# Optimization experiments

Hardware: AMD Instinct MI355X
Metric: run time of the kernel (lower is better)

Reference implementation:

```python
import jax, jax.numpy as jnp
import numpy as np

B, C, H, W = 16, 192, 56, 56
WS = 7; L = WS * WS; NH = 8; HD = C // NH
SHIFTS = (0, 3, 0, 3)  # shift = 0 if i%2==0 else window_size//2


def _ln(x, g, b):
    m = jnp.mean(x, -1, keepdims=True)
    v = jnp.var(x, -1, keepdims=True)
    return (x - m) * jax.lax.rsqrt(v + 1e-5) * g + b


def _win_part(x):
    # (b, H, W, c) -> (b*nW, L, c)
    b, c = x.shape[0], x.shape[-1]
    x = x.reshape(b, H // WS, WS, W // WS, WS, c).transpose(0, 1, 3, 2, 4, 5)
    return x.reshape(-1, L, c)


def _win_rev(xw, b):
    # (b*nW, L, c) -> (b, H, W, c)
    c = xw.shape[-1]
    x = xw.reshape(b, H // WS, W // WS, WS, WS, c).transpose(0, 1, 3, 2, 4, 5)
    return x.reshape(b, H, W, c)


def _rel_index():
    co = np.stack(np.meshgrid(np.arange(WS), np.arange(WS), indexing='ij')).reshape(2, -1)
    r = (co[:, :, None] - co[:, None, :]).transpose(1, 2, 0).astype(np.int64)
    r[..., 0] += WS - 1; r[..., 1] += WS - 1; r[..., 0] *= 2 * WS - 1
    return r.sum(-1)  # (L, L)

REL_IDX = _rel_index()


def _mask(shift):
    if shift == 0:
        return None
    img = np.zeros((1, H, W, 1), np.float32)
    cnt = 0.0
    sl = (slice(0, H - WS), slice(H - WS, H - shift), slice(H - shift, None))
    for hs in sl:
        for ws_ in sl:
            img[:, hs, ws_, :] = cnt
            cnt += 1.0
    mw = np.asarray(_win_part(jnp.asarray(img))).reshape(-1, L)
    am = mw[:, None, :] - mw[:, :, None]
    return jnp.asarray(np.where(am != 0, -100.0, 0.0).astype(np.float32))  # (nW, L, L)

MASKS = [_mask(s) for s in SHIFTS]


def _block(x, n1g, n1b, qw, qb, pw, pb, tab, n2g, n2b, f1w, f1b, f2w, f2b, shift, mask):
    b = x.shape[0]
    sc = x
    x = _ln(x, n1g, n1b)
    if shift:
        x = jnp.roll(x, (-shift, -shift), (1, 2))
    xw = _win_part(x)  # (b*nW, L, C)
    qkv = (xw @ qw.T + qb).reshape(-1, L, 3, NH, HD).transpose(2, 0, 3, 1, 4)
    q, k, v = qkv[0], qkv[1], qkv[2]  # (nB, NH, L, HD)
    attn = jnp.einsum('bhid,bhjd->bhij', q * (HD ** -0.5), k)
    attn = attn + tab[REL_IDX].transpose(2, 0, 1)  # relative position bias (NH, L, L)
    if mask is not None:
        nW = mask.shape[0]
        attn = (attn.reshape(b, nW, NH, L, L) + mask[None, :, None]).reshape(-1, NH, L, L)
    attn = jax.nn.softmax(attn, -1)
    out = jnp.einsum('bhij,bhjd->bhid', attn, v).transpose(0, 2, 1, 3).reshape(-1, L, C)
    out = out @ pw.T + pb
    x = _win_rev(out, b)
    if shift:
        x = jnp.roll(x, (shift, shift), (1, 2))
    x = sc + x
    y = _ln(x, n2g, n2b)
    y = jax.nn.gelu(y @ f1w.T + f1b, approximate=False) @ f2w.T + f2b
    return x + y


def _conv_bn_relu(x, w, b, g, bt, m, v):
    x = jax.lax.conv_general_dilated(x, w, (1, 1), ((1, 1), (1, 1)),
                                     dimension_numbers=('NCHW', 'OIHW', 'NCHW'))
    x = x + b[None, :, None, None]
    x = (x - m[None, :, None, None]) * jax.lax.rsqrt(v + 1e-5)[None, :, None, None]
    x = x * g[None, :, None, None] + bt[None, :, None, None]
    return jax.nn.relu(x)


def setup_inputs() -> dict:
    key = jax.random.key(0)
    ks = iter(jax.random.split(key, 48))
    rn = lambda shape, s=0.02: jax.random.normal(next(ks), shape, jnp.float32) * s
    OD = 96
    return dict(
        x=jax.random.normal(next(ks), (B, C, H, W), jnp.float32),
        pos_embed=rn((1, H * W, C)),
        proj_w=rn((C, C)), proj_b=jnp.zeros((C,)),
        pe_g=jnp.ones((C,)), pe_b=jnp.zeros((C,)),
        n1_g=jnp.ones((4, C)), n1_b=jnp.zeros((4, C)),
        qkv_w=rn((4, 3 * C, C)), qkv_b=jnp.zeros((4, 3 * C)),
        attn_pw=rn((4, C, C)), attn_pb=jnp.zeros((4, C)),
        rel_tab=rn((4, (2 * WS - 1) ** 2, NH)),
        n2_g=jnp.ones((4, C)), n2_b=jnp.zeros((4, C)),
        fc1_w=rn((4, 4 * C, C)), fc1_b=jnp.zeros((4, 4 * C)),
        fc2_w=rn((4, C, 4 * C)), fc2_b=jnp.zeros((4, C)),
        c1_w=rn((C, C, 3, 3)), c1_b=jnp.zeros((C,)),
        bn1_g=jnp.ones((C,)), bn1_b=jnp.zeros((C,)), bn1_m=rn((C,), 0.1), bn1_v=jnp.ones((C,)),
        c2_w=rn((OD, C, 3, 3)), c2_b=jnp.zeros((OD,)),
        bn2_g=jnp.ones((OD,)), bn2_b=jnp.zeros((OD,)), bn2_m=rn((OD,), 0.1), bn2_v=jnp.ones((OD,)),
    )


def reference(x, pos_embed, proj_w, proj_b, pe_g, pe_b, n1_g, n1_b, qkv_w, qkv_b,
              attn_pw, attn_pb, rel_tab, n2_g, n2_b, fc1_w, fc1_b, fc2_w, fc2_b,
              c1_w, c1_b, bn1_g, bn1_b, bn1_m, bn1_v,
              c2_w, c2_b, bn2_g, bn2_b, bn2_m, bn2_v):
    # PatchEmbedding: 1x1 conv == per-pixel linear, then LN, + pos embed
    t = jnp.einsum('bchw,dc->bhwd', x, proj_w) + proj_b  # (B, H, W, D)
    t = _ln(t.reshape(B, H * W, C), pe_g, pe_b) + pos_embed
    o = t.reshape(B, H, W, C)
    for i in range(4):
        o = _block(o, n1_g[i], n1_b[i], qkv_w[i], qkv_b[i], attn_pw[i], attn_pb[i],
                   rel_tab[i], n2_g[i], n2_b[i], fc1_w[i], fc1_b[i], fc2_w[i], fc2_b[i],
                   SHIFTS[i], MASKS[i])
    ds2 = o.transpose(0, 3, 1, 2)  # (B, C, H, W)
    h1 = _conv_bn_relu(ds2, c1_w, c1_b, bn1_g, bn1_b, bn1_m, bn1_v)
    conv_out = _conv_bn_relu(h1, c2_w, c2_b, bn2_g, bn2_b, bn2_m, bn2_v)
    return (conv_out, ds2)
```

## Files before the change

### kernel.cpp

```cpp
#include <hip/hip_runtime.h>
#include <math.h>

typedef unsigned short u16;
typedef unsigned int u32;
typedef __attribute__((ext_vector_type(8))) short short8;
typedef __attribute__((ext_vector_type(4))) float f32x4;

#define IMG 56
#define HW_ 3136
#define NTOK 50176
#define C_DIM 192
#define CONV_OUT_SZ 4816896

#define SZ_QKV (4*576*192)
#define SZ_FC1 (4*768*192)
#define SZ_FC2 (4*192*768)
#define SZ_PW  (4*192*192)
#define SZ_PROJ (192*192)
#define SZ_C1R (192*1728)
#define SZ_C2R (128*1728)

__device__ inline float bf2f(u16 v) {
  u32 u = ((u32)v) << 16; float f; __builtin_memcpy(&f, &u, 4); return f;
}
__device__ inline u16 f2bf(float f) {
  u32 u; __builtin_memcpy(&u, &f, 4);
  u += 0x7FFF + ((u >> 16) & 1);
  return (u16)(u >> 16);
}
__device__ inline void glds16(const u16* g, u16* l) {
  __builtin_amdgcn_global_load_lds((const __attribute__((address_space(1))) u32*)g,
                                   (__attribute__((address_space(3))) u32*)l, 16, 0, 0);
}
__device__ inline u32 pk_bf16(float a, float b) {
  u32 r;
  asm("v_cvt_pk_bf16_f32 %0, %1, %2" : "=v"(r) : "v"(a), "v"(b));
  return r;
}

__device__ inline void xcd_decode(int f, int NB, int& mb, int& nb) {
  const int ml = f & 7;
  const int rest = f >> 3;
  nb = rest % NB;
  mb = (rest / NB) * 8 + ml;
}

template<int AMODE, int EPI>
__global__ __launch_bounds__(256) void gmm(
    const u16* __restrict__ A, const u16* __restrict__ W,
    const float* __restrict__ bias, void* __restrict__ Cout,
    int M, int N, int K, int NB,
    const float* __restrict__ bg, const float* __restrict__ bb,
    const float* __restrict__ bm, const float* __restrict__ bv, int shiftp)
{
  __shared__ u16 As[128 * 64];
  __shared__ u16 Bs[64 * 64];
  const int tid = threadIdx.x;
  int mb, nb;
  xcd_decode(blockIdx.x, NB, mb, nb);
  const int m0 = mb * 128, n0 = nb * 64;
  const int lane = tid & 63, wid = tid >> 6;
  const int wm = (wid >> 1) * 64, wn = (wid & 1) * 32;
  const int fr = lane & 15, fg = lane >> 4;
  f32x4 acc[4][2] = {};

  const u16* rowp0; const u16* rowp1; const u16* rowp2; const u16* rowp3;
  int ry0, ry1, ry2, ry3, rx0, rx1, rx2, rx3;
  if (AMODE == 1) {
    #pragma unroll
    for (int it = 0; it < 4; ++it) {
      const int g = it * 256 + tid;
      const int row = g >> 3;
      const int m = m0 + row;
      const int b = m / HW_, pp = m - b * HW_;
      const int y = pp / IMG, x = pp - (pp / IMG) * IMG;
      const u16* rp = A + ((size_t)(b * HW_ + y * IMG + x)) * C_DIM;
      if (it == 0) { rowp0 = rp; ry0 = y; rx0 = x; }
      else if (it == 1) { rowp1 = rp; ry1 = y; rx1 = x; }
      else if (it == 2) { rowp2 = rp; ry2 = y; rx2 = x; }
      else { rowp3 = rp; ry3 = y; rx3 = x; }
    }
  }

  for (int kc = 0; kc < K; kc += 64) {
    #pragma unroll
    for (int it = 0; it < 2; ++it) {
      const int g = it * 256 + tid;
      const int row = g >> 3, cb = (g & 7) << 4;
      const int sc = cb ^ ((row & 7) << 4);
      glds16(W + (size_t)(n0 + row) * K + kc + (sc >> 1), Bs + g * 8);
    }
    if (AMODE == 0) {
      #pragma unroll
      for (int it = 0; it < 4; ++it) {
        const int g = it * 256 + tid;
        const int row = g >> 3, cb = (g & 7) << 4;
        const int sc = cb ^ ((row & 7) << 4);
        glds16(A + (size_t)(m0 + row) * K + kc + (sc >> 1), As + g * 8);
      }
    } else {
      #pragma unroll
      for (int it = 0; it < 4; ++it) {
        const int g = it * 256 + tid;
        const int row = g >> 3, cb = (g & 7) << 4;
        const int kg = kc + (cb >> 1);
        const int s = kg / C_DIM, ic = kg - s * C_DIM;
        const int dy = s / 3 - 1, dx = s % 3 - 1;
        const u16* rp = (it == 0) ? rowp0 : (it == 1) ? rowp1 : (it == 2) ? rowp2 : rowp3;
        const int y = (it == 0) ? ry0 : (it == 1) ? ry1 : (it == 2) ? ry2 : ry3;
        const int x = (it == 0) ? rx0 : (it == 1) ? rx1 : (it == 2) ? rx2 : rx3;
        const int yy = y + dy, xx = x + dx;
        short8 v = {0, 0, 0, 0, 0, 0, 0, 0};
        if ((unsigned)yy < IMG && (unsigned)xx < IMG)
          v = *(const short8*)(rp + (dy * IMG + dx) * C_DIM + ic);
        *(short8*)(As + row * 64 + ((cb ^ ((row & 7) << 4)) >> 1)) = v;
      }
    }
    __syncthreads();
    #pragma unroll
    for (int ks = 0; ks < 2; ++ks) {
      const int kb = ks * 64 + fg * 16;
      short8 af[4], bfv[2];
      #pragma unroll
      for (int i = 0; i < 4; ++i) {
        const int row = wm + i * 16 + fr;
        af[i] = *(const short8*)(As + ((row * 128 + (kb ^ ((row & 7) << 4))) >> 1));
      }
      #pragma unroll
      for (int j = 0; j < 2; ++j) {
        const int row = wn + j * 16 + fr;
        bfv[j] = *(const short8*)(Bs + ((row * 128 + (kb ^ ((row & 7) << 4))) >> 1));
      }
      #pragma unroll
      for (int i = 0; i < 4; ++i)
        #pragma unroll
        for (int j = 0; j < 2; ++j)
          acc[i][j] = __builtin_amdgcn_mfma_f32_16x16x32_bf16(af[i], bfv[j], acc[i][j], 0, 0, 0);
    }
    __syncthreads();
  }

  const int c0 = n0 + wn + fr;
  const int c1i = (EPI == 4) ? min(c0 + 16, N - 1) : (c0 + 16);
  const float bias0 = bias[c0], bias1 = bias[c1i];
  float s0 = 0.f, h0 = 0.f, s1 = 0.f, h1 = 0.f;
  if (EPI == 3 || EPI == 4) {
    s0 = bg[c0] * rsqrtf(bv[c0] + 1e-5f); h0 = bb[c0] - bm[c0] * s0;
    s1 = bg[c1i] * rsqrtf(bv[c1i] + 1e-5f); h1 = bb[c1i] - bm[c1i] * s1;
  }

  if (EPI == 0 || EPI == 1 || EPI == 2 || EPI == 6) {
    #pragma unroll
    for (int i = 0; i < 4; ++i) {
      #pragma unroll
      for (int r = 0; r < 4; ++r) {
        const int ml = wm + i * 16 + fg * 4 + r;
        #pragma unroll
        for (int j = 0; j < 2; ++j) {
          float v = acc[i][j][r] + (j ? bias1 : bias0);
          if (EPI == 1) v = 0.5f * v * (1.f + erff(v * 0.70710678118f));
          const int cl = wn + j * 16 + fr;
          As[ml * 64 + ((cl & 7) | ((((cl >> 3) ^ ml) & 7) << 3))] = f2bf(v);
        }
      }
    }
    __syncthreads();
    #pragma unroll
    for (int p = 0; p < 4; ++p) {
      const int id = p * 256 + tid;
      const int ml = id >> 3, grp = id & 7;
      const int pg = (grp ^ ml) & 7;
      const short8 vv = *(const short8*)(As + ml * 64 + pg * 8);
      if (EPI == 0 || EPI == 1) {
        *(short8*)((u16*)Cout + (size_t)(m0 + ml) * N + n0 + grp * 8) = vv;
      } else {
        size_t dstoff;
        if (EPI == 2) {
          dstoff = (size_t)(m0 + ml) * N + n0 + grp * 8;
        } else {
          const int m = m0 + ml;
          const int wno = m / 49, within = m - wno * 49;
          const int b2 = wno >> 6, wb3 = wno & 63;
          const int wr = within / 7, wc = within - wr * 7;
          int y2 = (wb3 >> 3) * 7 + wr + shiftp; if (y2 >= IMG) y2 -= IMG;
          int x2 = (wb3 & 7) * 7 + wc + shiftp; if (x2 >= IMG) x2 -= IMG;
          dstoff = ((size_t)(b2 * HW_ + y2 * IMG + x2)) * C_DIM + n0 + grp * 8;
        }
        u16* p8 = (u16*)Cout + dstoff;
        const short8 old = *(const short8*)p8;
        const u16* av_ = (const u16*)&vv;
        const u16* ov_ = (const u16*)&old;
        u32 res[4];
        #pragma unroll
        for (int e = 0; e < 4; ++e)
          res[e] = pk_bf16(bf2f(ov_[2 * e]) + bf2f(av_[2 * e]),
                           bf2f(ov_[2 * e + 1]) + bf2f(av_[2 * e + 1]));
        *(short8*)p8 = *(const short8*)res;
      }
    }
  } else {
    #pragma unroll
    for (int i = 0; i < 4; ++i) {
      #pragma unroll
      for (int r = 0; r < 4; ++r) {
        const int m = m0 + wm + i * 16 + fg * 4 + r;
        #pragma unroll
        for (int j = 0; j < 2; ++j) {
          const int c = c0 + j * 16;
          float v = acc[i][j][r] + (j ? bias1 : bias0);
          v = v * (j ? s1 : s0) + (j ? h1 : h0);
          v = fmaxf(v, 0.f);
          if (EPI == 3) {
            ((u16*)Cout)[(size_t)m * N + c] = f2bf(v);
          } else {
            if (c < N) {
              const int b = m / HW_, pp = m - b * HW_;
              ((float*)Cout)[((size_t)b * N + c) * HW_ + pp] = v;
            }
          }
        }
      }
    }
  }
}

template<int EPI>
__global__ __launch_bounds__(256) void gmm64(
    const u16* __restrict__ A, const u16* __restrict__ W,
    const float* __restrict__ bias, void* __restrict__ Cout,
    int M, int N, int K, int NB, int shiftp)
{
  __shared__ u16 As[64 * 64];
  __shared__ u16 Bs[64 * 64];
  const int tid = threadIdx.x;
  int mb, nb;
  xcd_decode(blockIdx.x, NB, mb, nb);
  const int m0 = mb * 64, n0 = nb * 64;
  const int lane = tid & 63, wid = tid >> 6;
  const int wm = (wid >> 1) * 32, wn = (wid & 1) * 32;
  const int fr = lane & 15, fg = lane >> 4;
  f32x4 acc[2][2] = {};

  for (int kc = 0; kc < K; kc += 64) {
    #pragma unroll
    for (int it = 0; it < 2; ++it) {
      const int g = it * 256 + tid;
      const int row = g >> 3, cb = (g & 7) << 4;
      const int sc = cb ^ ((row & 7) << 4);
      glds16(W + (size_t)(n0 + row) * K + kc + (sc >> 1), Bs + g * 8);
      glds16(A + (size_t)(m0 + row) * K + kc + (sc >> 1), As + g * 8);
    }
    __syncthreads();
    #pragma unroll
    for (int ks = 0; ks < 2; ++ks) {
      const int kb = ks * 64 + fg * 16;
      short8 af[2], bfv[2];
      #pragma unroll
      for (int i = 0; i < 2; ++i) {
        const int row = wm + i * 16 + fr;
        af[i] = *(const short8*)(As + ((row * 128 + (kb ^ ((row & 7) << 4))) >> 1));
      }
      #pragma unroll
      for (int j = 0; j < 2; ++j) {
        const int row = wn + j * 16 + fr;
        bfv[j] = *(const short8*)(Bs + ((row * 128 + (kb ^ ((row & 7) << 4))) >> 1));
      }
      #pragma unroll
      for (int i = 0; i < 2; ++i)
        #pragma unroll
        for (int j = 0; j < 2; ++j)
          acc[i][j] = __builtin_amdgcn_mfma_f32_16x16x32_bf16(af[i], bfv[j], acc[i][j], 0, 0, 0);
    }
    __syncthreads();
  }

  const int c0 = n0 + wn + fr;
  const float bias0 = bias[c0], bias1 = bias[c0 + 16];
  #pragma unroll
  for (int i = 0; i < 2; ++i) {
    #pragma unroll
    for (int r = 0; r < 4; ++r) {
      const int ml = wm + i * 16 + fg * 4 + r;
      #pragma unroll
      for (int j = 0; j < 2; ++j) {
        const float v = acc[i][j][r] + (j ? bias1 : bias0);
        const int cl = wn + j * 16 + fr;
        As[ml * 64 + ((cl & 7) | ((((cl >> 3) ^ ml) & 7) << 3))] = f2bf(v);
      }
    }
  }
  __syncthreads();
  #pragma unroll
  for (int p = 0; p < 2; ++p) {
    const int id = p * 256 + tid;
    const int ml = id >> 3, grp = id & 7;
    const int pg = (grp ^ ml) & 7;
    const short8 vv = *(const short8*)(As + ml * 64 + pg * 8);
    if (EPI == 0) {
      *(short8*)((u16*)Cout + (size_t)(m0 + ml) * N + n0 + grp * 8) = vv;
    } else {
      const int m = m0 + ml;
      const int wno = m / 49, within = m - wno * 49;
      const int b2 = wno >> 6, wb3 = wno & 63;
      const int wr = within / 7, wc = within - wr * 7;
      int y2 = (wb3 >> 3) * 7 + wr + shiftp; if (y2 >= IMG) y2 -= IMG;
      int x2 = (wb3 & 7) * 7 + wc + shiftp; if (x2 >= IMG) x2 -= IMG;
      const size_t dstoff = ((size_t)(b2 * HW_ + y2 * IMG + x2)) * C_DIM + n0 + grp * 8;
      u16* p8 = (u16*)Cout + dstoff;
      const short8 old = *(const short8*)p8;
      const u16* av_ = (const u16*)&vv;
      const u16* ov_ = (const u16*)&old;
      u32 res[4];
      #pragma unroll
      for (int e = 0; e < 4; ++e)
        res[e] = pk_bf16(bf2f(ov_[2 * e]) + bf2f(av_[2 * e]),
                         bf2f(ov_[2 * e + 1]) + bf2f(av_[2 * e + 1]));
      *(short8*)p8 = *(const short8*)res;
    }
  }
}

__global__ __launch_bounds__(256) void ln_k(
    const u16* __restrict__ in, u16* __restrict__ outp,
    const float* __restrict__ g, const float* __restrict__ bta,
    const float* __restrict__ pos, int winpart, int shift)
{
  const int t = blockIdx.x * 4 + (threadIdx.x >> 6);
  const int lane = threadIdx.x & 63;
  const uint2* row = (const uint2*)(in + (size_t)t * C_DIM);
  uint2 w = make_uint2(0, 0);
  if (lane < 48) w = row[lane];
  const float v0 = bf2f((u16)w.x), v1 = bf2f(w.x >> 16);
  const float v2 = bf2f((u16)w.y), v3 = bf2f(w.y >> 16);
  float s = v0 + v1 + v2 + v3;
  float ss = v0 * v0 + v1 * v1 + v2 * v2 + v3 * v3;
  #pragma unroll
  for (int off = 32; off > 0; off >>= 1) {
    s += __shfl_xor(s, off);
    ss += __shfl_xor(ss, off);
  }
  const float mean = s * (1.f / 192.f);
  const float inv = rsqrtf(ss * (1.f / 192.f) - mean * mean + 1e-5f);
  const int b = t / HW_, pp = t - b * HW_;
  size_t obase;
  if (winpart) {
    const int y = pp / IMG, x = pp - (pp / IMG) * IMG;
    int yr = y - shift; if (yr < 0) yr += IMG;
    int xs = x - shift; if (xs < 0) xs += IMG;
    const int win = b * 64 + (yr / 7) * 8 + (xs / 7);
    const int within = (yr % 7) * 7 + (xs % 7);
    obase = ((size_t)win * 49 + within) * C_DIM;
  } else {
    obase = (size_t)t * C_DIM;
  }
  if (lane < 48) {
    const float4 gg = *(const float4*)(g + lane * 4);
    const float4 bb = *(const float4*)(bta + lane * 4);
    float p0 = 0.f, p1 = 0.f, p2 = 0.f, p3 = 0.f;
    if (pos) {
      const float4 pv = *(const float4*)(pos + (size_t)pp * C_DIM + lane * 4);
      p0 = pv.x; p1 = pv.y; p2 = pv.z; p3 = pv.w;
    }
    const float r0 = (v0 - mean) * inv * gg.x + bb.x + p0;
    const float r1 = (v1 - mean) * inv * gg.y + bb.y + p1;
    const float r2 = (v2 - mean) * inv * gg.z + bb.z + p2;
    const float r3 = (v3 - mean) * inv * gg.w + bb.w + p3;
    ((uint2*)(outp + obase))[lane] = make_uint2(pk_bf16(r0, r1), pk_bf16(r2, r3));
  }
}

template<int SHIFT>
__global__ __launch_bounds__(256) void attn_m(
    const u16* __restrict__ qkv, u16* __restrict__ outp,
    const float* __restrict__ rel)
{
  __shared__ u16 VT[128 * 64];
  __shared__ float relS[4 * 176 + 16];
  const int tid = threadIdx.x;
  const int wid = tid >> 6, lane = tid & 63;
  const int fr = lane & 15, fg = lane >> 4;
  const int win = blockIdx.x >> 1;
  const int hb = blockIdx.x & 1;
  const int h = hb * 4 + wid;
  const u16* wbase = qkv + (size_t)win * 49 * 576;

  {
    u32* vz = (u32*)VT;
    #pragma unroll
    for (int it = 0; it < 16; ++it) vz[it * 256 + tid] = 0;
  }
  for (int id = tid; id < 169 * 4; id += 256) {
    const int hl = id & 3, ridx = id >> 2;
    relS[hl * 176 + ridx] = rel[ridx * 8 + hb * 4 + hl];
  }
  __syncthreads();
  for (int id = tid; id < 49 * 24; id += 256) {
    const int j = id / 24, dq = id - (id / 24) * 24;
    const int dd = dq * 4;
    const uint2 v = *(const uint2*)(wbase + j * 576 + 384 + hb * 96 + dd);
    const u16* pv = (const u16*)&v;
    const int wpr = dd / 24, dl = dd - wpr * 24;
    #pragma unroll
    for (int e = 0; e < 4; ++e) {
      const int row = wpr * 32 + dl + e;
      VT[(row * 128 + ((j * 2) ^ (((row >> 2) & 7) << 4))) >> 1] = pv[e];
    }
  }
  __syncthreads();

  short8 qf[4], kf[4];
  #pragma unroll
  for (int t = 0; t < 4; ++t) {
    const int row = t * 16 + fr;
    if (fg < 3) {
      qf[t] = *(const short8*)(wbase + row * 576 + h * 24 + fg * 8);
      kf[t] = *(const short8*)(wbase + row * 576 + 192 + h * 24 + fg * 8);
    } else {
      qf[t] = (short8){0, 0, 0, 0, 0, 0, 0, 0};
      kf[t] = (short8){0, 0, 0, 0, 0, 0, 0, 0};
    }
  }

  short8 av[2][2];
  #pragma unroll
  for (int db = 0; db < 2; ++db) {
    const int row = wid * 32 + db * 16 + fr;
    const int swz = ((row >> 2) & 7) << 4;
    #pragma unroll
    for (int ks = 0; ks < 2; ++ks) {
      const uint2 lo = *(const uint2*)((const char*)VT + row * 128 + (((2 * ks) * 32 + fg * 8) ^ swz));
      const uint2 hi = *(const uint2*)((const char*)VT + row * 128 + (((2 * ks + 1) * 32 + fg * 8) ^ swz));
      u32 w[4] = {lo.x, lo.y, hi.x, hi.y};
      av[db][ks] = *(short8*)w;
    }
  }

  const int wb2 = win & 63;
  const int hblk = wb2 >> 3, wblk = wb2 & 7;

  u32 joffPk[4];
  u32 jregPk[2] = {0, 0};
  #pragma unroll
  for (int nj = 0; nj < 4; ++nj) {
    u32 w = 0;
    #pragma unroll
    for (int r = 0; r < 4; ++r) {
      const int j = nj * 16 + fg * 4 + r;
      const int r2 = j / 7, c2 = j - r2 * 7;
      w |= (u32)(r2 * 13 + c2) << (r * 8);
      if (SHIFT) {
        const int hj = hblk * 7 + r2, wj = wblk * 7 + c2;
        const int rj = (hj < 49 ? 0 : (hj < 53 ? 1 : 2)) * 3 + (wj < 49 ? 0 : (wj < 53 ? 1 : 2));
        jregPk[nj >> 1] |= (u32)rj << (((nj & 1) * 4 + r) * 4);
      }
    }
    joffPk[nj] = w;
  }

  const float* relw = relS + wid * 176;
  const float scl = 0.20412414523193154f;

  #pragma unroll
  for (int mi = 0; mi < 4; ++mi) {
    f32x4 sacc[4];
    #pragma unroll
    for (int nj = 0; nj < 4; ++nj)
      sacc[nj] = __builtin_amdgcn_mfma_f32_16x16x32_bf16(kf[nj], qf[mi],
                                                         (f32x4){0, 0, 0, 0}, 0, 0, 0);
    const int i = mi * 16 + fr;
    const int r1 = i / 7, c1 = i - r1 * 7;
    const int base13 = (r1 + 6) * 13 + (c1 + 6);
    int ri = 0;
    if (SHIFT) {
      const int hi2 = hblk * 7 + r1, wi2 = wblk * 7 + c1;
      ri = (hi2 < 49 ? 0 : (hi2 < 53 ? 1 : 2)) * 3 + (wi2 < 49 ? 0 : (wi2 < 53 ? 1 : 2));
    }
    float p[16];
    float mx = -1e30f;
    #pragma unroll
    for (int nj = 0; nj < 4; ++nj) {
      #pragma unroll
      for (int r = 0; r < 4; ++r) {
        const int j = nj * 16 + fg * 4 + r;
        int idx = base13 - (int)((joffPk[nj] >> (r * 8)) & 0xff);
        idx = min(max(idx, 0), 168);
        float v = sacc[nj][r] * scl + relw[idx];
        if (SHIFT) {
          const int rj = (jregPk[nj >> 1] >> (((nj & 1) * 4 + r) * 4)) & 0xf;
          v = (ri != rj) ? v - 100.f : v;
        }
        v = (j < 49) ? v : -1e30f;
        p[nj * 4 + r] = v;
        mx = fmaxf(mx, v);
      }
    }
    mx = fmaxf(mx, __shfl_xor(mx, 16));
    mx = fmaxf(mx, __shfl_xor(mx, 32));
    float sum = 0.f;
    #pragma unroll
    for (int e = 0; e < 16; ++e) { p[e] = __expf(p[e] - mx); sum += p[e]; }
    sum += __shfl_xor(sum, 16);
    sum += __shfl_xor(sum, 32);
    const float inv = 1.f / sum;
    short8 pb[2];
    #pragma unroll
    for (int ks = 0; ks < 2; ++ks) {
      u32 w[4];
      #pragma unroll
      for (int half = 0; half < 2; ++half) {
        const int nj = 2 * ks + half;
        w[half * 2 + 0] = pk_bf16(p[nj * 4 + 0] * inv, p[nj * 4 + 1] * inv);
        w[half * 2 + 1] = pk_bf16(p[nj * 4 + 2] * inv, p[nj * 4 + 3] * inv);
      }
      pb[ks] = *(short8*)w;
    }
    f32x4 o0 = {0, 0, 0, 0}, o1 = {0, 0, 0, 0};
    o0 = __builtin_amdgcn_mfma_f32_16x16x32_bf16(av[0][0], pb[0], o0, 0, 0, 0);
    o0 = __builtin_amdgcn_mfma_f32_16x16x32_bf16(av[0][1], pb[1], o0, 0, 0, 0);
    o1 = __builtin_amdgcn_mfma_f32_16x16x32_bf16(av[1][0], pb[0], o1, 0, 0, 0);
    o1 = __builtin_amdgcn_mfma_f32_16x16x32_bf16(av[1][1], pb[1], o1, 0, 0, 0);
    if (i < 49) {
      u16* orow = outp + ((size_t)win * 49 + i) * C_DIM + h * 24;
      *(uint2*)(orow + fg * 4) =
          make_uint2(pk_bf16(o0[0], o0[1]), pk_bf16(o0[2], o0[3]));
      if (fg < 2)
        *(uint2*)(orow + 16 + fg * 4) =
            make_uint2(pk_bf16(o1[0], o1[1]), pk_bf16(o1[2], o1[3]));
    }
  }
}

__global__ __launch_bounds__(256) void transpose_k(
    const u16* __restrict__ in, float* __restrict__ outp)
{
  __shared__ float tile[32][33];
  const int p0 = blockIdx.x * 32;
  const int c0 = blockIdx.y * 32;
  const int tid = threadIdx.x;
  #pragma unroll
  for (int it = 0; it < 2; ++it) {
    const int id = tid + it * 256;
    const int r = id >> 4, c2 = id & 15;
    const u32 v = *(const u32*)(in + (size_t)(p0 + r) * C_DIM + c0 + c2 * 2);
    tile[r][c2 * 2] = bf2f((u16)v);
    tile[r][c2 * 2 + 1] = bf2f(v >> 16);
  }
  __syncthreads();
  const int b = p0 / HW_, pp0 = p0 - b * HW_;
  #pragma unroll
  for (int it = 0; it < 4; ++it) {
    const int id = tid + it * 256;
    const int cl = id >> 5, pl = id & 31;
    outp[((size_t)b * C_DIM + c0 + cl) * HW_ + pp0 + pl] = tile[pl][cl];
  }
}

__global__ __launch_bounds__(256) void tok_k(
    const float* __restrict__ in, u16* __restrict__ outp)
{
  __shared__ float tile[32][33];
  const int t0 = blockIdx.x * 32;
  const int c0 = blockIdx.y * 32;
  const int tid = threadIdx.x;
  const int b = t0 / HW_, p0 = t0 - b * HW_;
  #pragma unroll
  for (int it = 0; it < 4; ++it) {
    const int id = tid + it * 256;
    const int cl = id >> 5, pl = id & 31;
    tile[cl][pl] = in[((size_t)b * C_DIM + c0 + cl) * HW_ + p0 + pl];
  }
  __syncthreads();
  #pragma unroll
  for (int it = 0; it < 4; ++it) {
    const int id = tid + it * 256;
    const int r = id >> 5, cc = id & 31;
    outp[(size_t)(t0 + r) * C_DIM + c0 + cc] = f2bf(tile[cc][r]);
  }
}

__global__ __launch_bounds__(256) void cvtall_k(
    const float* __restrict__ qkv_w, const float* __restrict__ fc1_w,
    const float* __restrict__ fc2_w, const float* __restrict__ attn_pw,
    const float* __restrict__ proj_w, const float* __restrict__ c1_w,
    const float* __restrict__ c2_w, u16* __restrict__ wbf)
{
  const int i = blockIdx.x * 256 + threadIdx.x;
  const int off1 = SZ_QKV, off2 = off1 + SZ_FC1, off3 = off2 + SZ_FC2,
            off4 = off3 + SZ_PW, off5 = off4 + SZ_PROJ, off6 = off5 + SZ_C1R,
            off7 = off6 + SZ_C2R;
  if (i >= off7) return;
  float v;
  if (i < off1) v = qkv_w[i];
  else if (i < off2) v = fc1_w[i - off1];
  else if (i < off3) v = fc2_w[i - off2];
  else if (i < off4) v = attn_pw[i - off3];
  else if (i < off5) v = proj_w[i - off4];
  else if (i < off6) {
    const int e = i - off5;
    const int n = e / 1728, kkk = e - n * 1728;
    const int s = kkk / C_DIM, ic = kkk - s * C_DIM;
    v = c1_w[((size_t)n * C_DIM + ic) * 9 + s];
  } else {
    const int e = i - off6;
    const int n = e / 1728, kkk = e - n * 1728;
    const int s = kkk / C_DIM, ic = kkk - s * C_DIM;
    v = (n < 96) ? c2_w[((size_t)n * C_DIM + ic) * 9 + s] : 0.f;
  }
  wbf[i] = f2bf(v);
}

extern "C" void kernel_launch(void* const* d_in, const int* in_sizes, int n_in,
                              void* d_out, int out_size, void* d_ws, size_t ws_size,
                              hipStream_t stream)
{
  const float* x       = (const float*)d_in[0];
  const float* pos     = (const float*)d_in[1];
  const float* proj_w  = (const float*)d_in[2];
  const float* proj_b  = (const float*)d_in[3];
  const float* pe_g    = (const float*)d_in[4];
  const float* pe_b    = (const float*)d_in[5];
  const float* n1_g    = (const float*)d_in[6];
  const float* n1_b    = (const float*)d_in[7];
  const float* qkv_w   = (const float*)d_in[8];
  const float* qkv_b   = (const float*)d_in[9];
  const float* attn_pw = (const float*)d_in[10];
  const float* attn_pb = (const float*)d_in[11];
  const float* rel_tab = (const float*)d_in[12];
  const float* n2_g    = (const float*)d_in[13];
  const float* n2_b    = (const float*)d_in[14];
  const float* fc1_w   = (const float*)d_in[15];
  const float* fc1_b   = (const float*)d_in[16];
  const float* fc2_w   = (const float*)d_in[17];
  const float* fc2_b   = (const float*)d_in[18];
  const float* c1_w    = (const float*)d_in[19];
  const float* c1_b    = (const float*)d_in[20];
  const float* bn1_g   = (const float*)d_in[21];
  const float* bn1_b   = (const float*)d_in[22];
  const float* bn1_m   = (const float*)d_in[23];
  const float* bn1_v   = (const float*)d_in[24];
  const float* c2_w    = (const float*)d_in[25];
  const float* c2_b    = (const float*)d_in[26];
  const float* bn2_g   = (const float*)d_in[27];
  const float* bn2_b   = (const float*)d_in[28];
  const float* bn2_m   = (const float*)d_in[29];
  const float* bn2_v   = (const float*)d_in[30];
  float* out = (float*)d_out;

  const size_t ACTB = (size_t)NTOK * C_DIM * 2;
  const size_t BIGB = (size_t)NTOK * 768 * 2;
  char* ws = (char*)d_ws;
  u16* act   = (u16*)ws;
  u16* big16 = (u16*)(ws + ACTB);
  u16* xln   = (u16*)(ws + ACTB + BIGB);
  u16* attn_out = (u16*)d_out;
  u16* wbf = (u16*)((char*)d_out + (size_t)CONV_OUT_SZ * 4);

  const size_t O_QKV = 0;
  const size_t O_FC1 = O_QKV + SZ_QKV;
  const size_t O_FC2 = O_FC1 + SZ_FC1;
  const size_t O_PW  = O_FC2 + SZ_FC2;
  const size_t O_PROJ= O_PW  + SZ_PW;
  const size_t O_C1  = O_PROJ+ SZ_PROJ;
  const size_t O_C2  = O_C1  + SZ_C1R;

  const dim3 blk(256);

  const int cvtall_n = SZ_QKV + SZ_FC1 + SZ_FC2 + SZ_PW + SZ_PROJ + SZ_C1R + SZ_C2R;
  cvtall_k<<<(cvtall_n + 255) / 256, blk, 0, stream>>>(
      qkv_w, fc1_w, fc2_w, attn_pw, proj_w, c1_w, c2_w, wbf);

  tok_k<<<dim3(1568, 6), blk, 0, stream>>>(x, xln);
  gmm64<0><<<dim3(784 * 3), blk, 0, stream>>>(
      xln, wbf + O_PROJ, proj_b, big16, NTOK, 192, 192, 3, 0);
  ln_k<<<12544, blk, 0, stream>>>(big16, act, pe_g, pe_b, pos, 0, 0);

  for (int i = 0; i < 4; ++i) {
    const int shift = (i & 1) ? 3 : 0;
    ln_k<<<12544, blk, 0, stream>>>(act, xln, n1_g + i * 192, n1_b + i * 192,
                                    nullptr, 1, shift);
    gmm<0, 0><<<dim3(392 * 9), blk, 0, stream>>>(
        xln, wbf + O_QKV + (size_t)i * 576 * 192, qkv_b + i * 576, big16,
        NTOK, 576, 192, 9, nullptr, nullptr, nullptr, nullptr, 0);
    if (shift)
      attn_m<3><<<2048, blk, 0, stream>>>(big16, attn_out, rel_tab + i * 169 * 8);
    else
      attn_m<0><<<2048, blk, 0, stream>>>(big16, attn_out, rel_tab + i * 169 * 8);
    gmm64<6><<<dim3(784 * 3), blk, 0, stream>>>(
        attn_out, wbf + O_PW + (size_t)i * 192 * 192, attn_pb + i * 192, act,
        NTOK, 192, 192, 3, shift);
    ln_k<<<12544, blk, 0, stream>>>(act, xln, n2_g + i * 192, n2_b + i * 192,
                                    nullptr, 0, 0);
    gmm<0, 1><<<dim3(392 * 12), blk, 0, stream>>>(
        xln, wbf + O_FC1 + (size_t)i * 768 * 192, fc1_b + i * 768, big16,
        NTOK, 768, 192, 12, nullptr, nullptr, nullptr, nullptr, 0);
    gmm<0, 2><<<dim3(392 * 3), blk, 0, stream>>>(
        big16, wbf + O_FC2 + (size_t)i * 192 * 768, fc2_b + i * 192, act,
        NTOK, 192, 768, 3, nullptr, nullptr, nullptr, nullptr, 0);
  }

  gmm<1, 3><<<dim3(392 * 3), blk, 0, stream>>>(
      act, wbf + O_C1, c1_b, big16, NTOK, 192, 1728, 3, bn1_g, bn1_b, bn1_m, bn1_v, 0);
  gmm<1, 4><<<dim3(392 * 2), blk, 0, stream>>>(
      big16, wbf + O_C2, c2_b, out, NTOK, 96, 1728, 2, bn2_g, bn2_b, bn2_m, bn2_v, 0);
  transpose_k<<<dim3(1568, 6), blk, 0, stream>>>(act, out + CONV_OUT_SZ);
}
```

Measured before the change: 828.3 us.

## Loop over N tiles inside gmm64 blocks and route QKV/FC1/FC2 through it

The 64x64 GEMM kernel now has each block own one 64-row M strip and loop serially over every N tile, so the grid shrinks to 784 blocks. The aim is to keep that A strip hot in cache across N tiles. The QKV, FC1 (with GELU) and FC2 (with residual add) GEMMs move from the larger-tile gmm kernel to this one, and gmm keeps only its conv/BN epilogues. The trade-off is smaller MFMA tiles, serial N loops with no overlap between tiles, and fewer blocks in flight to hide latency.

```diff
diff --git a/kernel.cpp b/kernel.cpp
--- a/kernel.cpp
+++ b/kernel.cpp
@@ -143,15 +143,89 @@
   const int c0 = n0 + wn + fr;
   const int c1i = (EPI == 4) ? min(c0 + 16, N - 1) : (c0 + 16);
   const float bias0 = bias[c0], bias1 = bias[c1i];
-  float s0 = 0.f, h0 = 0.f, s1 = 0.f, h1 = 0.f;
-  if (EPI == 3 || EPI == 4) {
-    s0 = bg[c0] * rsqrtf(bv[c0] + 1e-5f); h0 = bb[c0] - bm[c0] * s0;
-    s1 = bg[c1i] * rsqrtf(bv[c1i] + 1e-5f); h1 = bb[c1i] - bm[c1i] * s1;
-  }
-
-  if (EPI == 0 || EPI == 1 || EPI == 2 || EPI == 6) {
-    #pragma unroll
-    for (int i = 0; i < 4; ++i) {
+  const float s0 = bg[c0] * rsqrtf(bv[c0] + 1e-5f);
+  const float h0 = bb[c0] - bm[c0] * s0;
+  const float s1 = bg[c1i] * rsqrtf(bv[c1i] + 1e-5f);
+  const float h1 = bb[c1i] - bm[c1i] * s1;
+
+  #pragma unroll
+  for (int i = 0; i < 4; ++i) {
+    #pragma unroll
+    for (int r = 0; r < 4; ++r) {
+      const int m = m0 + wm + i * 16 + fg * 4 + r;
+      #pragma unroll
+      for (int j = 0; j < 2; ++j) {
+        const int c = c0 + j * 16;
+        float v = acc[i][j][r] + (j ? bias1 : bias0);
+        v = v * (j ? s1 : s0) + (j ? h1 : h0);
+        v = fmaxf(v, 0.f);
+        if (EPI == 3) {
+          ((u16*)Cout)[(size_t)m * N + c] = f2bf(v);
+        } else {
+          if (c < N) {
+            const int b = m / HW_, pp = m - b * HW_;
+            ((float*)Cout)[((size_t)b * N + c) * HW_ + pp] = v;
+          }
+        }
+      }
+    }
+  }
+}
+
+template<int EPI>
+__global__ __launch_bounds__(256) void gmm64(
+    const u16* __restrict__ A, const u16* __restrict__ W,
+    const float* __restrict__ bias, void* __restrict__ Cout,
+    int M, int N, int K, int NLOOP, int shiftp)
+{
+  __shared__ u16 As[64 * 64];
+  __shared__ u16 Bs[64 * 64];
+  const int tid = threadIdx.x;
+  const int m0 = blockIdx.x * 64;
+  const int lane = tid & 63, wid = tid >> 6;
+  const int wm = (wid >> 1) * 32, wn = (wid & 1) * 32;
+  const int fr = lane & 15, fg = lane >> 4;
+
+  for (int nb2 = 0; nb2 < NLOOP; ++nb2) {
+    const int n0 = nb2 * 64;
+    f32x4 acc[2][2] = {};
+    for (int kc = 0; kc < K; kc += 64) {
+      #pragma unroll
+      for (int it = 0; it < 2; ++it) {
+        const int g = it * 256 + tid;
+        const int row = g >> 3, cb = (g & 7) << 4;
+        const int sc = cb ^ ((row & 7) << 4);
+        glds16(W + (size_t)(n0 + row) * K + kc + (sc >> 1), Bs + g * 8);
+        glds16(A + (size_t)(m0 + row) * K + kc + (sc >> 1), As + g * 8);
+      }
+      __syncthreads();
+      #pragma unroll
+      for (int ks = 0; ks < 2; ++ks) {
+        const int kb = ks * 64 + fg * 16;
+        short8 af[2], bfv[2];
+        #pragma unroll
+        for (int i = 0; i < 2; ++i) {
+          const int row = wm + i * 16 + fr;
+          af[i] = *(const short8*)(As + ((row * 128 + (kb ^ ((row & 7) << 4))) >> 1));
+        }
+        #pragma unroll
+        for (int j = 0; j < 2; ++j) {
+          const int row = wn + j * 16 + fr;
+          bfv[j] = *(const short8*)(Bs + ((row * 128 + (kb ^ ((row & 7) << 4))) >> 1));
+        }
+        #pragma unroll
+        for (int i = 0; i < 2; ++i)
+          #pragma unroll
+          for (int j = 0; j < 2; ++j)
+            acc[i][j] = __builtin_amdgcn_mfma_f32_16x16x32_bf16(af[i], bfv[j], acc[i][j], 0, 0, 0);
+      }
+      __syncthreads();
+    }
+
+    const int c0 = n0 + wn + fr;
+    const float bias0 = bias[c0], bias1 = bias[c0 + 16];
+    #pragma unroll
+    for (int i = 0; i < 2; ++i) {
       #pragma unroll
       for (int r = 0; r < 4; ++r) {
         const int ml = wm + i * 16 + fg * 4 + r;
@@ -166,7 +240,7 @@
     }
     __syncthreads();
     #pragma unroll
-    for (int p = 0; p < 4; ++p) {
+    for (int p = 0; p < 2; ++p) {
       const int id = p * 256 + tid;
       const int ml = id >> 3, grp = id & 7;
       const int pg = (grp ^ ml) & 7;
@@ -198,125 +272,7 @@
         *(short8*)p8 = *(const short8*)res;
       }
     }
-  } else {
-    #pragma unroll
-    for (int i = 0; i < 4; ++i) {
-      #pragma unroll
-      for (int r = 0; r < 4; ++r) {
-        const int m = m0 + wm + i * 16 + fg * 4 + r;
-        #pragma unroll
-        for (int j = 0; j < 2; ++j) {
-          const int c = c0 + j * 16;
-          float v = acc[i][j][r] + (j ? bias1 : bias0);
-          v = v * (j ? s1 : s0) + (j ? h1 : h0);
-          v = fmaxf(v, 0.f);
-          if (EPI == 3) {
-            ((u16*)Cout)[(size_t)m * N + c] = f2bf(v);
-          } else {
-            if (c < N) {
-              const int b = m / HW_, pp = m - b * HW_;
-              ((float*)Cout)[((size_t)b * N + c) * HW_ + pp] = v;
-            }
-          }
-        }
-      }
-    }
-  }
-}
-
-template<int EPI>
-__global__ __launch_bounds__(256) void gmm64(
-    const u16* __restrict__ A, const u16* __restrict__ W,
-    const float* __restrict__ bias, void* __restrict__ Cout,
-    int M, int N, int K, int NB, int shiftp)
-{
-  __shared__ u16 As[64 * 64];
-  __shared__ u16 Bs[64 * 64];
-  const int tid = threadIdx.x;
-  int mb, nb;
-  xcd_decode(blockIdx.x, NB, mb, nb);
-  const int m0 = mb * 64, n0 = nb * 64;
-  const int lane = tid & 63, wid = tid >> 6;
-  const int wm = (wid >> 1) * 32, wn = (wid & 1) * 32;
-  const int fr = lane & 15, fg = lane >> 4;
-  f32x4 acc[2][2] = {};
-
-  for (int kc = 0; kc < K; kc += 64) {
-    #pragma unroll
-    for (int it = 0; it < 2; ++it) {
-      const int g = it * 256 + tid;
-      const int row = g >> 3, cb = (g & 7) << 4;
-      const int sc = cb ^ ((row & 7) << 4);
-      glds16(W + (size_t)(n0 + row) * K + kc + (sc >> 1), Bs + g * 8);
-      glds16(A + (size_t)(m0 + row) * K + kc + (sc >> 1), As + g * 8);
-    }
     __syncthreads();
-    #pragma unroll
-    for (int ks = 0; ks < 2; ++ks) {
-      const int kb = ks * 64 + fg * 16;
-      short8 af[2], bfv[2];
-      #pragma unroll
-      for (int i = 0; i < 2; ++i) {
-        const int row = wm + i * 16 + fr;
-        af[i] = *(const short8*)(As + ((row * 128 + (kb ^ ((row & 7) << 4))) >> 1));
-      }
-      #pragma unroll
-      for (int j = 0; j < 2; ++j) {
-        const int row = wn + j * 16 + fr;
-        bfv[j] = *(const short8*)(Bs + ((row * 128 + (kb ^ ((row & 7) << 4))) >> 1));
-      }
-      #pragma unroll
-      for (int i = 0; i < 2; ++i)
-        #pragma unroll
-        for (int j = 0; j < 2; ++j)
-          acc[i][j] = __builtin_amdgcn_mfma_f32_16x16x32_bf16(af[i], bfv[j], acc[i][j], 0, 0, 0);
-    }
-    __syncthreads();
-  }
-
-  const int c0 = n0 + wn + fr;
-  const float bias0 = bias[c0], bias1 = bias[c0 + 16];
-  #pragma unroll
-  for (int i = 0; i < 2; ++i) {
-    #pragma unroll
-    for (int r = 0; r < 4; ++r) {
-      const int ml = wm + i * 16 + fg * 4 + r;
-      #pragma unroll
-      for (int j = 0; j < 2; ++j) {
-        const float v = acc[i][j][r] + (j ? bias1 : bias0);
-        const int cl = wn + j * 16 + fr;
-        As[ml * 64 + ((cl & 7) | ((((cl >> 3) ^ ml) & 7) << 3))] = f2bf(v);
-      }
-    }
-  }
-  __syncthreads();
-  #pragma unroll
-  for (int p = 0; p < 2; ++p) {
-    const int id = p * 256 + tid;
-    const int ml = id >> 3, grp = id & 7;
-    const int pg = (grp ^ ml) & 7;
-    const short8 vv = *(const short8*)(As + ml * 64 + pg * 8);
-    if (EPI == 0) {
-      *(short8*)((u16*)Cout + (size_t)(m0 + ml) * N + n0 + grp * 8) = vv;
-    } else {
-      const int m = m0 + ml;
-      const int wno = m / 49, within = m - wno * 49;
-      const int b2 = wno >> 6, wb3 = wno & 63;
-      const int wr = within / 7, wc = within - wr * 7;
-      int y2 = (wb3 >> 3) * 7 + wr + shiftp; if (y2 >= IMG) y2 -= IMG;
-      int x2 = (wb3 & 7) * 7 + wc + shiftp; if (x2 >= IMG) x2 -= IMG;
-      const size_t dstoff = ((size_t)(b2 * HW_ + y2 * IMG + x2)) * C_DIM + n0 + grp * 8;
-      u16* p8 = (u16*)Cout + dstoff;
-      const short8 old = *(const short8*)p8;
-      const u16* av_ = (const u16*)&vv;
-      const u16* ov_ = (const u16*)&old;
-      u32 res[4];
-      #pragma unroll
-      for (int e = 0; e < 4; ++e)
-        res[e] = pk_bf16(bf2f(ov_[2 * e]) + bf2f(av_[2 * e]),
-                         bf2f(ov_[2 * e + 1]) + bf2f(av_[2 * e + 1]));
-      *(short8*)p8 = *(const short8*)res;
-    }
   }
 }
 
@@ -670,7 +626,7 @@
       qkv_w, fc1_w, fc2_w, attn_pw, proj_w, c1_w, c2_w, wbf);
 
   tok_k<<<dim3(1568, 6), blk, 0, stream>>>(x, xln);
-  gmm64<0><<<dim3(784 * 3), blk, 0, stream>>>(
+  gmm64<0><<<dim3(784), blk, 0, stream>>>(
       xln, wbf + O_PROJ, proj_b, big16, NTOK, 192, 192, 3, 0);
   ln_k<<<12544, blk, 0, stream>>>(big16, act, pe_g, pe_b, pos, 0, 0);
 
@@ -678,24 +634,24 @@
     const int shift = (i & 1) ? 3 : 0;
     ln_k<<<12544, blk, 0, stream>>>(act, xln, n1_g + i * 192, n1_b + i * 192,
                                     nullptr, 1, shift);
-    gmm<0, 0><<<dim3(392 * 9), blk, 0, stream>>>(
+    gmm64<0><<<dim3(784), blk, 0, stream>>>(
         xln, wbf + O_QKV + (size_t)i * 576 * 192, qkv_b + i * 576, big16,
-        NTOK, 576, 192, 9, nullptr, nullptr, nullptr, nullptr, 0);
+        NTOK, 576, 192, 9, 0);
     if (shift)
       attn_m<3><<<2048, blk, 0, stream>>>(big16, attn_out, rel_tab + i * 169 * 8);
     else
       attn_m<0><<<2048, blk, 0, stream>>>(big16, attn_out, rel_tab + i * 169 * 8);
-    gmm64<6><<<dim3(784 * 3), blk, 0, stream>>>(
+    gmm64<6><<<dim3(784), blk, 0, stream>>>(
         attn_out, wbf + O_PW + (size_t)i * 192 * 192, attn_pb + i * 192, act,
         NTOK, 192, 192, 3, shift);
     ln_k<<<12544, blk, 0, stream>>>(act, xln, n2_g + i * 192, n2_b + i * 192,
                                     nullptr, 0, 0);
-    gmm<0, 1><<<dim3(392 * 12), blk, 0, stream>>>(
+    gmm64<1><<<dim3(784), blk, 0, stream>>>(
         xln, wbf + O_FC1 + (size_t)i * 768 * 192, fc1_b + i * 768, big16,
-        NTOK, 768, 192, 12, nullptr, nullptr, nullptr, nullptr, 0);
-    gmm<0, 2><<<dim3(392 * 3), blk, 0, stream>>>(
+        NTOK, 768, 192, 12, 0);
+    gmm64<2><<<dim3(784), blk, 0, stream>>>(
         big16, wbf + O_FC2 + (size_t)i * 192 * 768, fc2_b + i * 192, act,
-        NTOK, 192, 768, 3, nullptr, nullptr, nullptr, nullptr, 0);
+        NTOK, 192, 768, 3, 0);
   }
 
   gmm<1, 3><<<dim3(392 * 3), blk, 0, stream>>>(
```

Measured after the change: 957.4 us. 15.6% more time.
